# Kernel optimization log

Measured on AMD Instinct MI355X. Metric: run time of the kernel, lower is better.

## Reference

```python
import jax, jax.numpy as jnp
import numpy as np


def _rope(v, pos, head_dim):
    # v: [H, D]; rotate consecutive pairs by angle pos * theta_j
    theta = 1.0 / (10000.0 ** (jnp.arange(0, head_dim, 2, dtype=jnp.float32) / head_dim))
    ang = pos * theta                      # [D/2]
    cos, sin = jnp.cos(ang), jnp.sin(ang)
    vr = v.reshape(v.shape[0], -1, 2)      # [H, D/2, 2]
    re = vr[..., 0] * cos - vr[..., 1] * sin
    im = vr[..., 0] * sin + vr[..., 1] * cos
    return jnp.stack([re, im], axis=-1).reshape(v.shape)


def setup_inputs() -> dict:
    key = jax.random.key(0)
    ks = jax.random.split(key, 7)
    dim, H, D, S = 4096, 32, 128, 2048
    scale = 0.02
    return {
        "x": jax.random.normal(ks[0], (dim,), dtype=jnp.float32),
        "wq": jax.random.normal(ks[1], (dim, dim), dtype=jnp.float32) * scale,
        "wk": jax.random.normal(ks[2], (dim, dim), dtype=jnp.float32) * scale,
        "wv": jax.random.normal(ks[3], (dim, dim), dtype=jnp.float32) * scale,
        "wo": jax.random.normal(ks[4], (dim, dim), dtype=jnp.float32) * scale,
        "cache_k": jax.random.normal(ks[5], (S, H, D), dtype=jnp.float32),
        "cache_v": jax.random.normal(ks[6], (S, H, D), dtype=jnp.float32),
        "pos": 1536,
    }


def reference(x, wq, wk, wv, wo, cache_k, cache_v, pos):
    H, D = cache_k.shape[1], cache_k.shape[2]
    # nn.Linear without bias: y = W @ x
    xq = (wq @ x).reshape(H, D)
    xk = (wk @ x).reshape(H, D)
    xv = (wv @ x).reshape(H, D)
    xq = _rope(xq, pos, D)
    xk = _rope(xk, pos, D)
    # KV cache append (pos is a static Python int)
    cache_k = cache_k.at[pos].set(xk)
    cache_v = cache_v.at[pos].set(xv)
    keys = cache_k[: pos + 1]              # [P, H, D]
    values = cache_v[: pos + 1]            # [P, H, D]
    # single-query decode attention per head
    scores = jnp.einsum("hd,phd->hp", xq, keys) / jnp.sqrt(jnp.float32(D))
    scores = jax.nn.softmax(scores, axis=-1)
    out = jnp.einsum("hp,phd->hd", scores, values)   # [H, D]
    return wo @ out.reshape(-1)
```

## Files before the change

kernel.cpp:

```cpp
#include <hip/hip_runtime.h>
#include <math.h>

#define DIM 4096
#define H 32
#define D 128
#define SMAX 2048
#define CHUNK 32
#define NCHUNK (SMAX / CHUNK)
#define PART_STRIDE 130

typedef float v4f __attribute__((ext_vector_type(4)));
typedef unsigned int u32;

__device__ __forceinline__ float wave_sum(float v) {
#pragma unroll
    for (int o = 32; o; o >>= 1) v += __shfl_xor(v, o);
    return v;
}

__device__ __forceinline__ void gload_lds16(const float* g, float* l) {
    __builtin_amdgcn_global_load_lds(
        (const __attribute__((address_space(1))) u32*)g,
        (__attribute__((address_space(3))) u32*)l, 16, 0, 0);
}

__global__ void __launch_bounds__(256) qk_rope(
        const float* __restrict__ wq, const float* __restrict__ wk,
        const float* __restrict__ x, const int* __restrict__ pos_p,
        float* __restrict__ xq, float* __restrict__ xk) {
    __shared__ float buf[2 * DIM];
    __shared__ float red[2][4];
    int t = threadIdx.x, lane = t & 63, w = t >> 6;
    int bid = blockIdx.x;
    bool isq = bid < 2048;
    int pr = bid & 2047;
    const float* base = (isq ? wq : wk) + (size_t)pr * 2 * DIM;

    v4f xr[4];
#pragma unroll
    for (int i = 0; i < 4; ++i)
        xr[i] = *reinterpret_cast<const v4f*>(x + i * 1024 + t * 4);

#pragma unroll
    for (int i = 0; i < 8; ++i)
        gload_lds16(base + i * 1024 + t * 4, &buf[i * 1024 + t * 4]);

    __syncthreads();

    float a0 = 0.f, a1 = 0.f, a2 = 0.f, a3 = 0.f;
    float b0 = 0.f, b1 = 0.f, b2 = 0.f, b3 = 0.f;
#pragma unroll
    for (int i = 0; i < 4; ++i) {
        v4f ra = *reinterpret_cast<v4f*>(&buf[i * 1024 + t * 4]);
        v4f rb = *reinterpret_cast<v4f*>(&buf[DIM + i * 1024 + t * 4]);
        a0 = fmaf(ra.x, xr[i].x, a0);
        a1 = fmaf(ra.y, xr[i].y, a1);
        a2 = fmaf(ra.z, xr[i].z, a2);
        a3 = fmaf(ra.w, xr[i].w, a3);
        b0 = fmaf(rb.x, xr[i].x, b0);
        b1 = fmaf(rb.y, xr[i].y, b1);
        b2 = fmaf(rb.z, xr[i].z, b2);
        b3 = fmaf(rb.w, xr[i].w, b3);
    }
    float da = wave_sum((a0 + a1) + (a2 + a3));
    float db = wave_sum((b0 + b1) + (b2 + b3));
    if (lane == 0) { red[0][w] = da; red[1][w] = db; }
    __syncthreads();
    if (t == 0) {
        float d0 = red[0][0] + red[0][1] + red[0][2] + red[0][3];
        float d1 = red[1][0] + red[1][1] + red[1][2] + red[1][3];
        int pos = *pos_p;
        int j = pr & 63;
        float theta = powf(10000.0f, -(float)(2 * j) / (float)D);
        float ang = (float)pos * theta;
        float s, c;
        sincosf(ang, &s, &c);
        float* o = isq ? xq : xk;
        o[2 * pr]     = d0 * c - d1 * s;
        o[2 * pr + 1] = d0 * s + d1 * c;
    }
}

__global__ void __launch_bounds__(256) v_mat(
        const float* __restrict__ wv, const float* __restrict__ x,
        float* __restrict__ xv) {
    __shared__ float red[4];
    int row = blockIdx.x;
    const float* w = wv + (size_t)row * DIM;
    int t = threadIdx.x;
    float acc = 0.f;
#pragma unroll
    for (int i = 0; i < 4; ++i) {
        int idx = (i * 256 + t) * 4;
        const float4 a = *reinterpret_cast<const float4*>(w + idx);
        const float4 b = *reinterpret_cast<const float4*>(x + idx);
        acc = fmaf(a.x, b.x, acc);
        acc = fmaf(a.y, b.y, acc);
        acc = fmaf(a.z, b.z, acc);
        acc = fmaf(a.w, b.w, acc);
    }
#pragma unroll
    for (int off = 32; off; off >>= 1) acc += __shfl_xor(acc, off);
    if ((t & 63) == 0) red[t >> 6] = acc;
    __syncthreads();
    if (t == 0) xv[row] = red[0] + red[1] + red[2] + red[3];
}

__device__ __forceinline__ void load_half(v4f (&buf)[8], const float* __restrict__ wp, int off) {
#pragma unroll
    for (int i = 0; i < 8; ++i)
        buf[i] = *reinterpret_cast<const v4f*>(wp + i * 256 + off);
}

template <int XO>
__device__ __forceinline__ float dot_half(const v4f (&buf)[8], const v4f (&xr)[16]) {
    float s0 = 0.f, s1 = 0.f, s2 = 0.f, s3 = 0.f;
#pragma unroll
    for (int i = 0; i < 8; ++i) {
        s0 = fmaf(buf[i].x, xr[XO + i].x, s0);
        s1 = fmaf(buf[i].y, xr[XO + i].y, s1);
        s2 = fmaf(buf[i].z, xr[XO + i].z, s2);
        s3 = fmaf(buf[i].w, xr[XO + i].w, s3);
    }
    return (s0 + s1) + (s2 + s3);
}

#define SB() __builtin_amdgcn_sched_barrier(0)

__global__ void __launch_bounds__(256) matvec_o(
        const float* __restrict__ w_, const float* __restrict__ vin,
        float* __restrict__ y) {
    int t = threadIdx.x, lane = t & 63;
    int W = blockIdx.x * 4 + (t >> 6);
    int r0 = W * 2;
    int off = lane * 4;

    v4f xr[16];
#pragma unroll
    for (int i = 0; i < 16; ++i)
        xr[i] = *reinterpret_cast<const v4f*>(vin + i * 256 + off);

    const float* w0 = w_ + (size_t)r0 * DIM;
    v4f A[8], B[8];
    float d0, d1;
    load_half(A, w0, off);
    load_half(B, w0 + 2048, off);            SB();
    d0  = dot_half<0>(A, xr);
    load_half(A, w0 + DIM, off);             SB();
    d0 += dot_half<8>(B, xr);
    load_half(B, w0 + DIM + 2048, off);      SB();
    d1  = dot_half<0>(A, xr);
    d1 += dot_half<8>(B, xr);

    d0 = wave_sum(d0); d1 = wave_sum(d1);
    if (lane == 0) { y[r0] = d0; y[r0 + 1] = d1; }
}

__global__ void attn_partial(const float* __restrict__ cache_k, const float* __restrict__ cache_v,
                             const float* __restrict__ xq, const float* __restrict__ xk,
                             const float* __restrict__ xv, const int* __restrict__ pos_p,
                             float* __restrict__ partials) {
    __shared__ float lds_m[4], lds_l[4];
    __shared__ float lds_acc[4][128];
    int h = blockIdx.x;
    int c = blockIdx.y;
    int lane = threadIdx.x;
    int g  = lane >> 4;
    int gl = lane & 15;
    int pos = *pos_p;
    int base = c * CHUNK;
    int p1 = min(base + CHUNK, pos + 1);
    float* pp = partials + (size_t)(h * NCHUNK + c) * PART_STRIDE;

    if (base > pos) {
        if (lane == 0) { pp[0] = -INFINITY; pp[1] = 0.f; }
        reinterpret_cast<float2*>(pp + 2)[lane] = make_float2(0.f, 0.f);
        return;
    }

    const float4* qv = reinterpret_cast<const float4*>(xq + h * D + gl * 8);
    const float4 q0 = qv[0], q1 = qv[1];

    float m = -INFINITY, l = 0.f;
    float4 acc0 = make_float4(0.f, 0.f, 0.f, 0.f);
    float4 acc1 = make_float4(0.f, 0.f, 0.f, 0.f);

    for (int p = base + g; p < p1; p += 4) {
        const float* kp = (p == pos) ? (xk + h * D)
                                     : (cache_k + ((size_t)p * H + h) * D);
        const float4* kv4 = reinterpret_cast<const float4*>(kp + gl * 8);
        float4 k0 = kv4[0], k1 = kv4[1];
        float d = q0.x * k0.x + q0.y * k0.y + q0.z * k0.z + q0.w * k0.w
                + q1.x * k1.x + q1.y * k1.y + q1.z * k1.z + q1.w * k1.w;
        d += __shfl_xor(d, 1);
        d += __shfl_xor(d, 2);
        d += __shfl_xor(d, 4);
        d += __shfl_xor(d, 8);
        float s = d * 0.08838834764831845f;
        float mn = fmaxf(m, s);
        float corr = __expf(m - mn);
        float wgt  = __expf(s - mn);
        const float* vp = (p == pos) ? (xv + h * D)
                                     : (cache_v + ((size_t)p * H + h) * D);
        const float4* vv4 = reinterpret_cast<const float4*>(vp + gl * 8);
        float4 v0 = vv4[0], v1 = vv4[1];
        l = l * corr + wgt;
        acc0.x = fmaf(wgt, v0.x, acc0.x * corr);
        acc0.y = fmaf(wgt, v0.y, acc0.y * corr);
        acc0.z = fmaf(wgt, v0.z, acc0.z * corr);
        acc0.w = fmaf(wgt, v0.w, acc0.w * corr);
        acc1.x = fmaf(wgt, v1.x, acc1.x * corr);
        acc1.y = fmaf(wgt, v1.y, acc1.y * corr);
        acc1.z = fmaf(wgt, v1.z, acc1.z * corr);
        acc1.w = fmaf(wgt, v1.w, acc1.w * corr);
        m = mn;
    }

    if (gl == 0) { lds_m[g] = m; lds_l[g] = l; }
    *reinterpret_cast<float4*>(&lds_acc[g][gl * 8])     = acc0;
    *reinterpret_cast<float4*>(&lds_acc[g][gl * 8 + 4]) = acc1;
    __syncthreads();
    float M = fmaxf(fmaxf(lds_m[0], lds_m[1]), fmaxf(lds_m[2], lds_m[3]));
    float w0 = __expf(lds_m[0] - M);
    float w1 = __expf(lds_m[1] - M);
    float w2 = __expf(lds_m[2] - M);
    float w3 = __expf(lds_m[3] - M);
    float L  = w0 * lds_l[0] + w1 * lds_l[1] + w2 * lds_l[2] + w3 * lds_l[3];
    int d0 = 2 * lane;
    float s0 = w0 * lds_acc[0][d0]     + w1 * lds_acc[1][d0]
             + w2 * lds_acc[2][d0]     + w3 * lds_acc[3][d0];
    float s1 = w0 * lds_acc[0][d0 + 1] + w1 * lds_acc[1][d0 + 1]
             + w2 * lds_acc[2][d0 + 1] + w3 * lds_acc[3][d0 + 1];
    if (lane == 0) { pp[0] = M; pp[1] = L; }
    reinterpret_cast<float2*>(pp + 2)[lane] = make_float2(s0, s1);
}

__global__ void attn_combine(const float* __restrict__ partials, float* __restrict__ out_attn) {
    int h = blockIdx.x;
    int lane = threadIdx.x;
    float m = -INFINITY;
    for (int c = 0; c < NCHUNK; ++c)
        m = fmaxf(m, partials[(size_t)(h * NCHUNK + c) * PART_STRIDE]);
    float L = 0.f, a0 = 0.f, a1 = 0.f;
    for (int c = 0; c < NCHUNK; ++c) {
        const float* pp = partials + (size_t)(h * NCHUNK + c) * PART_STRIDE;
        float w = __expf(pp[0] - m);
        L += pp[1] * w;
        float2 a = reinterpret_cast<const float2*>(pp + 2)[lane];
        a0 += w * a.x;
        a1 += w * a.y;
    }
    float inv = 1.f / L;
    out_attn[h * D + 2 * lane]     = a0 * inv;
    out_attn[h * D + 2 * lane + 1] = a1 * inv;
}

extern "C" void kernel_launch(void* const* d_in, const int* in_sizes, int n_in,
                              void* d_out, int out_size, void* d_ws, size_t ws_size,
                              hipStream_t stream) {
    const float* x       = (const float*)d_in[0];
    const float* wq      = (const float*)d_in[1];
    const float* wk      = (const float*)d_in[2];
    const float* wv      = (const float*)d_in[3];
    const float* wo      = (const float*)d_in[4];
    const float* cache_k = (const float*)d_in[5];
    const float* cache_v = (const float*)d_in[6];
    const int*   pos     = (const int*)d_in[7];

    float* ws       = (float*)d_ws;
    float* xq       = ws;
    float* xk       = ws + DIM;
    float* xv       = ws + 2 * DIM;
    float* partials = ws + 3 * DIM;
    float* out_attn = partials + H * NCHUNK * PART_STRIDE;
    float* out      = (float*)d_out;

    qk_rope<<<4096, 256, 0, stream>>>(wq, wk, x, pos, xq, xk);
    v_mat<<<DIM, 256, 0, stream>>>(wv, x, xv);
    attn_partial<<<dim3(H, NCHUNK), 64, 0, stream>>>(cache_k, cache_v, xq, xk, xv, pos, partials);
    attn_combine<<<H, 64, 0, stream>>>(partials, out_attn);
    matvec_o<<<512, 256, 0, stream>>>(wo, out_attn, out);
}
```

Before: 78.56 us.

## Fuse decode pipeline into one cooperative persistent kernel with grid syncs

Replaces the five separate launches (QK-rope matvec, V matvec, attention partials, combine, output projection) with a single cooperative kernel of 1024 persistent blocks, with grid.sync between stages. The aim is to remove launch gaps and tail effects between stages. The partial layout is also moved so the accumulator sits at offset 0 and max/sum at 128/129. The change risks grid.sync overhead, lower occupancy under launch bounds, and a fallback to the old path if cooperative launch is unavailable.

Measured after the change: 78.79 us. No clear change (+0.3%).

```diff
diff --git a/kernel.cpp b/kernel.cpp
--- a/kernel.cpp
+++ b/kernel.cpp
@@ -1,5 +1,8 @@
 #include <hip/hip_runtime.h>
+#include <hip/hip_cooperative_groups.h>
 #include <math.h>
+
+namespace cg = cooperative_groups;
 
 #define DIM 4096
 #define H 32
@@ -7,7 +10,9 @@
 #define SMAX 2048
 #define CHUNK 32
 #define NCHUNK (SMAX / CHUNK)
-#define PART_STRIDE 130
+#define PART_STRIDE 132
+#define NBLK 1024
+#define NTHR 256
 
 typedef float v4f __attribute__((ext_vector_type(4)));
 typedef unsigned int u32;
@@ -16,6 +21,217 @@
 #pragma unroll
     for (int o = 32; o; o >>= 1) v += __shfl_xor(v, o);
     return v;
+}
+
+__device__ __forceinline__ void vsum1632(v4f& v) {
+#pragma unroll
+    for (int i = 0; i < 4; ++i) {
+        float f = v[i];
+        f += __shfl_xor(f, 16);
+        f += __shfl_xor(f, 32);
+        v[i] = f;
+    }
+}
+
+__global__ void __launch_bounds__(NTHR, 4) fused_decode(
+        const float* __restrict__ wq, const float* __restrict__ wk,
+        const float* __restrict__ wv, const float* __restrict__ wo,
+        const float* __restrict__ x,
+        const float* __restrict__ cache_k, const float* __restrict__ cache_v,
+        const int* __restrict__ pos_p,
+        float* __restrict__ xq, float* __restrict__ xk, float* __restrict__ xv,
+        float* __restrict__ partials, float* __restrict__ out_attn,
+        float* __restrict__ y) {
+    __shared__ float xs[DIM];
+    __shared__ float red[2][2][4];
+    cg::grid_group grid = cg::this_grid();
+
+    int t = threadIdx.x, lane = t & 63, w = t >> 6;
+    int bid = blockIdx.x;
+    int pos = *pos_p;
+
+#pragma unroll
+    for (int i = 0; i < 4; ++i)
+        *reinterpret_cast<v4f*>(&xs[(i * 256 + t) * 4]) =
+            *reinterpret_cast<const v4f*>(x + (i * 256 + t) * 4);
+    __syncthreads();
+
+    {
+        int par = 0;
+        for (int tp = bid; tp < 3 * 2048; tp += NBLK, par ^= 1) {
+            int mat = tp >> 11;
+            int pr  = tp & 2047;
+            const float* wm = (mat == 0) ? wq : ((mat == 1) ? wk : wv);
+            const float* base = wm + (size_t)pr * 2 * DIM;
+            v4f wa[4], wb[4];
+#pragma unroll
+            for (int i = 0; i < 4; ++i) {
+                wa[i] = *reinterpret_cast<const v4f*>(base + i * 1024 + t * 4);
+                wb[i] = *reinterpret_cast<const v4f*>(base + DIM + i * 1024 + t * 4);
+            }
+            float a0 = 0.f, a1 = 0.f, a2 = 0.f, a3 = 0.f;
+            float b0 = 0.f, b1 = 0.f, b2 = 0.f, b3 = 0.f;
+#pragma unroll
+            for (int i = 0; i < 4; ++i) {
+                v4f xr = *reinterpret_cast<const v4f*>(&xs[i * 1024 + t * 4]);
+                a0 = fmaf(wa[i].x, xr.x, a0);
+                a1 = fmaf(wa[i].y, xr.y, a1);
+                a2 = fmaf(wa[i].z, xr.z, a2);
+                a3 = fmaf(wa[i].w, xr.w, a3);
+                b0 = fmaf(wb[i].x, xr.x, b0);
+                b1 = fmaf(wb[i].y, xr.y, b1);
+                b2 = fmaf(wb[i].z, xr.z, b2);
+                b3 = fmaf(wb[i].w, xr.w, b3);
+            }
+            float da = wave_sum((a0 + a1) + (a2 + a3));
+            float db = wave_sum((b0 + b1) + (b2 + b3));
+            if (lane == 0) { red[par][0][w] = da; red[par][1][w] = db; }
+            __syncthreads();
+            if (t == 0) {
+                float d0 = red[par][0][0] + red[par][0][1] + red[par][0][2] + red[par][0][3];
+                float d1 = red[par][1][0] + red[par][1][1] + red[par][1][2] + red[par][1][3];
+                if (mat == 2) {
+                    xv[2 * pr] = d0; xv[2 * pr + 1] = d1;
+                } else {
+                    int j = pr & 63;
+                    float theta = powf(10000.0f, -(float)(2 * j) / (float)D);
+                    float ang = (float)pos * theta;
+                    float s, c;
+                    sincosf(ang, &s, &c);
+                    float* o = (mat == 0) ? xq : xk;
+                    o[2 * pr]     = d0 * c - d1 * s;
+                    o[2 * pr + 1] = d0 * s + d1 * c;
+                }
+            }
+        }
+    }
+    grid.sync();
+
+    {
+        int gid = bid * 4 + w;
+        int g = lane >> 4, gl = lane & 15;
+        for (int task = gid; task < H * NCHUNK; task += NBLK * 4) {
+            int h = task >> 6;
+            int c = task & 63;
+            int base_p = c * CHUNK;
+            float* pp = partials + (size_t)task * PART_STRIDE;
+
+            float m = -INFINITY, l = 0.f;
+            v4f acc0 = {0.f, 0.f, 0.f, 0.f}, acc1 = {0.f, 0.f, 0.f, 0.f};
+
+            if (base_p <= pos) {
+                v4f q0 = *reinterpret_cast<const v4f*>(xq + h * D + gl * 8);
+                v4f q1 = *reinterpret_cast<const v4f*>(xq + h * D + gl * 8 + 4);
+                int p1 = min(base_p + CHUNK, pos + 1);
+                for (int p = base_p + g; p < p1; p += 4) {
+                    const float* kp = (p == pos) ? (xk + h * D)
+                                                 : (cache_k + ((size_t)p * H + h) * D);
+                    v4f k0 = *reinterpret_cast<const v4f*>(kp + gl * 8);
+                    v4f k1 = *reinterpret_cast<const v4f*>(kp + gl * 8 + 4);
+                    float d = q0.x * k0.x + q0.y * k0.y + q0.z * k0.z + q0.w * k0.w
+                            + q1.x * k1.x + q1.y * k1.y + q1.z * k1.z + q1.w * k1.w;
+                    d += __shfl_xor(d, 1);
+                    d += __shfl_xor(d, 2);
+                    d += __shfl_xor(d, 4);
+                    d += __shfl_xor(d, 8);
+                    float s = d * 0.08838834764831845f;
+                    float mn = fmaxf(m, s);
+                    float corr = __expf(m - mn);
+                    float wgt  = __expf(s - mn);
+                    const float* vp = (p == pos) ? (xv + h * D)
+                                                 : (cache_v + ((size_t)p * H + h) * D);
+                    v4f v0 = *reinterpret_cast<const v4f*>(vp + gl * 8);
+                    v4f v1 = *reinterpret_cast<const v4f*>(vp + gl * 8 + 4);
+                    l = l * corr + wgt;
+                    acc0 = acc0 * corr + v0 * wgt;
+                    acc1 = acc1 * corr + v1 * wgt;
+                    m = mn;
+                }
+            }
+            float mm = fmaxf(m, __shfl_xor(m, 16));
+            float M  = fmaxf(mm, __shfl_xor(mm, 32));
+            float wg = (m == -INFINITY) ? 0.f : __expf(m - M);
+            float lw = l * wg;
+            lw += __shfl_xor(lw, 16);
+            lw += __shfl_xor(lw, 32);
+            acc0 = acc0 * wg;
+            acc1 = acc1 * wg;
+            vsum1632(acc0);
+            vsum1632(acc1);
+            if (lane == 0) { pp[128] = M; pp[129] = lw; }
+            if (lane < 16) {
+                *reinterpret_cast<v4f*>(pp + gl * 8)     = acc0;
+                *reinterpret_cast<v4f*>(pp + gl * 8 + 4) = acc1;
+            }
+        }
+    }
+    grid.sync();
+
+    {
+        int gid = bid * 4 + w;
+        if (gid < H) {
+            int h = gid;
+            float m = -INFINITY;
+            for (int c = 0; c < NCHUNK; ++c)
+                m = fmaxf(m, partials[(size_t)(h * NCHUNK + c) * PART_STRIDE + 128]);
+            float L = 0.f, a0 = 0.f, a1 = 0.f;
+            for (int c = 0; c < NCHUNK; ++c) {
+                const float* pp = partials + (size_t)(h * NCHUNK + c) * PART_STRIDE;
+                float mw = pp[128];
+                float wgt = (mw == -INFINITY) ? 0.f : __expf(mw - m);
+                L += pp[129] * wgt;
+                float2 a = *reinterpret_cast<const float2*>(pp + 2 * lane);
+                a0 += wgt * a.x;
+                a1 += wgt * a.y;
+            }
+            float inv = 1.f / L;
+            out_attn[h * D + 2 * lane]     = a0 * inv;
+            out_attn[h * D + 2 * lane + 1] = a1 * inv;
+        }
+    }
+    grid.sync();
+
+#pragma unroll
+    for (int i = 0; i < 4; ++i)
+        *reinterpret_cast<v4f*>(&xs[(i * 256 + t) * 4]) =
+            *reinterpret_cast<const v4f*>(out_attn + (i * 256 + t) * 4);
+    __syncthreads();
+    {
+        int par = 0;
+        for (int tp = bid; tp < 2048; tp += NBLK, par ^= 1) {
+            const float* base = wo + (size_t)tp * 2 * DIM;
+            v4f wa[4], wb[4];
+#pragma unroll
+            for (int i = 0; i < 4; ++i) {
+                wa[i] = *reinterpret_cast<const v4f*>(base + i * 1024 + t * 4);
+                wb[i] = *reinterpret_cast<const v4f*>(base + DIM + i * 1024 + t * 4);
+            }
+            float a0 = 0.f, a1 = 0.f, a2 = 0.f, a3 = 0.f;
+            float b0 = 0.f, b1 = 0.f, b2 = 0.f, b3 = 0.f;
+#pragma unroll
+            for (int i = 0; i < 4; ++i) {
+                v4f xr = *reinterpret_cast<const v4f*>(&xs[i * 1024 + t * 4]);
+                a0 = fmaf(wa[i].x, xr.x, a0);
+                a1 = fmaf(wa[i].y, xr.y, a1);
+                a2 = fmaf(wa[i].z, xr.z, a2);
+                a3 = fmaf(wa[i].w, xr.w, a3);
+                b0 = fmaf(wb[i].x, xr.x, b0);
+                b1 = fmaf(wb[i].y, xr.y, b1);
+                b2 = fmaf(wb[i].z, xr.z, b2);
+                b3 = fmaf(wb[i].w, xr.w, b3);
+            }
+            float da = wave_sum((a0 + a1) + (a2 + a3));
+            float db = wave_sum((b0 + b1) + (b2 + b3));
+            if (lane == 0) { red[par][0][w] = da; red[par][1][w] = db; }
+            __syncthreads();
+            if (t == 0) {
+                float d0 = red[par][0][0] + red[par][0][1] + red[par][0][2] + red[par][0][3];
+                float d1 = red[par][1][0] + red[par][1][1] + red[par][1][2] + red[par][1][3];
+                y[2 * tp]     = d0;
+                y[2 * tp + 1] = d1;
+            }
+        }
+    }
 }
 
 __device__ __forceinline__ void gload_lds16(const float* g, float* l) {
@@ -173,8 +389,8 @@
     float* pp = partials + (size_t)(h * NCHUNK + c) * PART_STRIDE;
 
     if (base > pos) {
-        if (lane == 0) { pp[0] = -INFINITY; pp[1] = 0.f; }
-        reinterpret_cast<float2*>(pp + 2)[lane] = make_float2(0.f, 0.f);
+        if (lane == 0) { pp[128] = -INFINITY; pp[129] = 0.f; }
+        reinterpret_cast<float2*>(pp)[lane] = make_float2(0.f, 0.f);
         return;
     }
 
@@ -231,8 +447,8 @@
              + w2 * lds_acc[2][d0]     + w3 * lds_acc[3][d0];
     float s1 = w0 * lds_acc[0][d0 + 1] + w1 * lds_acc[1][d0 + 1]
              + w2 * lds_acc[2][d0 + 1] + w3 * lds_acc[3][d0 + 1];
-    if (lane == 0) { pp[0] = M; pp[1] = L; }
-    reinterpret_cast<float2*>(pp + 2)[lane] = make_float2(s0, s1);
+    if (lane == 0) { pp[128] = M; pp[129] = L; }
+    reinterpret_cast<float2*>(pp)[lane] = make_float2(s0, s1);
 }
 
 __global__ void attn_combine(const float* __restrict__ partials, float* __restrict__ out_attn) {
@@ -240,13 +456,14 @@
     int lane = threadIdx.x;
     float m = -INFINITY;
     for (int c = 0; c < NCHUNK; ++c)
-        m = fmaxf(m, partials[(size_t)(h * NCHUNK + c) * PART_STRIDE]);
+        m = fmaxf(m, partials[(size_t)(h * NCHUNK + c) * PART_STRIDE + 128]);
     float L = 0.f, a0 = 0.f, a1 = 0.f;
     for (int c = 0; c < NCHUNK; ++c) {
         const float* pp = partials + (size_t)(h * NCHUNK + c) * PART_STRIDE;
-        float w = __expf(pp[0] - m);
-        L += pp[1] * w;
-        float2 a = reinterpret_cast<const float2*>(pp + 2)[lane];
+        float mw = pp[128];
+        float w = (mw == -INFINITY) ? 0.f : __expf(mw - m);
+        L += pp[129] * w;
+        float2 a = *reinterpret_cast<const float2*>(pp + 2 * lane);
         a0 += w * a.x;
         a1 += w * a.y;
     }
@@ -267,17 +484,36 @@
     const float* cache_v = (const float*)d_in[6];
     const int*   pos     = (const int*)d_in[7];
 
-    float* ws       = (float*)d_ws;
-    float* xq       = ws;
-    float* xk       = ws + DIM;
-    float* xv       = ws + 2 * DIM;
-    float* partials = ws + 3 * DIM;
+    float* wsf      = (float*)d_ws;
+    float* xq       = wsf;
+    float* xk       = wsf + DIM;
+    float* xv       = wsf + 2 * DIM;
+    float* partials = wsf + 3 * DIM;
     float* out_attn = partials + H * NCHUNK * PART_STRIDE;
-    float* out      = (float*)d_out;
+    float* y        = (float*)d_out;
+
+    int dev = 0;
+    hipGetDevice(&dev);
+    int coop_ok = 0, n_cu = 0, occ = 0;
+    hipDeviceGetAttribute(&coop_ok, hipDeviceAttributeCooperativeLaunch, dev);
+    hipDeviceGetAttribute(&n_cu, hipDeviceAttributeMultiprocessorCount, dev);
+    hipOccupancyMaxActiveBlocksPerMultiprocessor(&occ, fused_decode, NTHR, 0);
+
+    if (coop_ok && occ > 0 && (long)occ * n_cu >= NBLK) {
+        void* args[] = {
+            (void*)&wq, (void*)&wk, (void*)&wv, (void*)&wo, (void*)&x,
+            (void*)&cache_k, (void*)&cache_v, (void*)&pos,
+            (void*)&xq, (void*)&xk, (void*)&xv,
+            (void*)&partials, (void*)&out_attn, (void*)&y
+        };
+        hipError_t e = hipLaunchCooperativeKernel((const void*)fused_decode,
+                                                  dim3(NBLK), dim3(NTHR), args, 0, stream);
+        if (e == hipSuccess) return;
+    }
 
     qk_rope<<<4096, 256, 0, stream>>>(wq, wk, x, pos, xq, xk);
     v_mat<<<DIM, 256, 0, stream>>>(wv, x, xv);
     attn_partial<<<dim3(H, NCHUNK), 64, 0, stream>>>(cache_k, cache_v, xq, xk, xv, pos, partials);
     attn_combine<<<H, 64, 0, stream>>>(partials, out_attn);
-    matvec_o<<<512, 256, 0, stream>>>(wo, out_attn, out);
-}
+    matvec_o<<<512, 256, 0, stream>>>(wo, out_attn, y);
+}
```

## Fuse Q/K/V projections into one launch and realign attention partial layout

Applied to the files above, without the earlier changes.

Merges the V projection into the Q/K RoPE kernel, so one launch of 6144 blocks covers all three weight matrices, with two rows per block. Weights now go through direct global vector loads instead of the asynchronous global-to-LDS copy and shared buffer. The attention partial record is padded to 132 floats, with the accumulator first and max/sum stored after it, so the float2 accesses stay aligned. The combine step now skips chunks whose max is -inf. This removes a kernel launch and the LDS staging overhead, but loses the LDS prefetch path and any overlap it provided.

Measured after the change: 80.59 us. +2.6%, slower.

```diff
diff --git a/kernel.cpp b/kernel.cpp
--- a/kernel.cpp
+++ b/kernel.cpp
@@ -7,10 +7,9 @@
 #define SMAX 2048
 #define CHUNK 32
 #define NCHUNK (SMAX / CHUNK)
-#define PART_STRIDE 130
+#define PART_STRIDE 132
 
 typedef float v4f __attribute__((ext_vector_type(4)));
-typedef unsigned int u32;
 
 __device__ __forceinline__ float wave_sum(float v) {
 #pragma unroll
@@ -18,49 +17,35 @@
     return v;
 }
 
-__device__ __forceinline__ void gload_lds16(const float* g, float* l) {
-    __builtin_amdgcn_global_load_lds(
-        (const __attribute__((address_space(1))) u32*)g,
-        (__attribute__((address_space(3))) u32*)l, 16, 0, 0);
-}
-
-__global__ void __launch_bounds__(256) qk_rope(
+__global__ void __launch_bounds__(256) qkv_rope(
         const float* __restrict__ wq, const float* __restrict__ wk,
-        const float* __restrict__ x, const int* __restrict__ pos_p,
-        float* __restrict__ xq, float* __restrict__ xk) {
-    __shared__ float buf[2 * DIM];
+        const float* __restrict__ wv, const float* __restrict__ x,
+        const int* __restrict__ pos_p,
+        float* __restrict__ xq, float* __restrict__ xk, float* __restrict__ xv) {
     __shared__ float red[2][4];
     int t = threadIdx.x, lane = t & 63, w = t >> 6;
-    int bid = blockIdx.x;
-    bool isq = bid < 2048;
-    int pr = bid & 2047;
-    const float* base = (isq ? wq : wk) + (size_t)pr * 2 * DIM;
-
-    v4f xr[4];
-#pragma unroll
-    for (int i = 0; i < 4; ++i)
-        xr[i] = *reinterpret_cast<const v4f*>(x + i * 1024 + t * 4);
-
-#pragma unroll
-    for (int i = 0; i < 8; ++i)
-        gload_lds16(base + i * 1024 + t * 4, &buf[i * 1024 + t * 4]);
-
-    __syncthreads();
+    int b = blockIdx.x;
+    int mat = b >> 11;
+    int pr  = b & 2047;
+    const float* wm = (mat == 0) ? wq : ((mat == 1) ? wk : wv);
+    const float* base = wm + (size_t)pr * 2 * DIM;
 
     float a0 = 0.f, a1 = 0.f, a2 = 0.f, a3 = 0.f;
     float b0 = 0.f, b1 = 0.f, b2 = 0.f, b3 = 0.f;
 #pragma unroll
     for (int i = 0; i < 4; ++i) {
-        v4f ra = *reinterpret_cast<v4f*>(&buf[i * 1024 + t * 4]);
-        v4f rb = *reinterpret_cast<v4f*>(&buf[DIM + i * 1024 + t * 4]);
-        a0 = fmaf(ra.x, xr[i].x, a0);
-        a1 = fmaf(ra.y, xr[i].y, a1);
-        a2 = fmaf(ra.z, xr[i].z, a2);
-        a3 = fmaf(ra.w, xr[i].w, a3);
-        b0 = fmaf(rb.x, xr[i].x, b0);
-        b1 = fmaf(rb.y, xr[i].y, b1);
-        b2 = fmaf(rb.z, xr[i].z, b2);
-        b3 = fmaf(rb.w, xr[i].w, b3);
+        int idx = i * 1024 + t * 4;
+        v4f wa = *reinterpret_cast<const v4f*>(base + idx);
+        v4f wb = *reinterpret_cast<const v4f*>(base + DIM + idx);
+        v4f xr = *reinterpret_cast<const v4f*>(x + idx);
+        a0 = fmaf(wa.x, xr.x, a0);
+        a1 = fmaf(wa.y, xr.y, a1);
+        a2 = fmaf(wa.z, xr.z, a2);
+        a3 = fmaf(wa.w, xr.w, a3);
+        b0 = fmaf(wb.x, xr.x, b0);
+        b1 = fmaf(wb.y, xr.y, b1);
+        b2 = fmaf(wb.z, xr.z, b2);
+        b3 = fmaf(wb.w, xr.w, b3);
     }
     float da = wave_sum((a0 + a1) + (a2 + a3));
     float db = wave_sum((b0 + b1) + (b2 + b3));
@@ -69,91 +54,20 @@
     if (t == 0) {
         float d0 = red[0][0] + red[0][1] + red[0][2] + red[0][3];
         float d1 = red[1][0] + red[1][1] + red[1][2] + red[1][3];
-        int pos = *pos_p;
-        int j = pr & 63;
-        float theta = powf(10000.0f, -(float)(2 * j) / (float)D);
-        float ang = (float)pos * theta;
-        float s, c;
-        sincosf(ang, &s, &c);
-        float* o = isq ? xq : xk;
-        o[2 * pr]     = d0 * c - d1 * s;
-        o[2 * pr + 1] = d0 * s + d1 * c;
-    }
-}
-
-__global__ void __launch_bounds__(256) v_mat(
-        const float* __restrict__ wv, const float* __restrict__ x,
-        float* __restrict__ xv) {
-    __shared__ float red[4];
-    int row = blockIdx.x;
-    const float* w = wv + (size_t)row * DIM;
-    int t = threadIdx.x;
-    float acc = 0.f;
-#pragma unroll
-    for (int i = 0; i < 4; ++i) {
-        int idx = (i * 256 + t) * 4;
-        const float4 a = *reinterpret_cast<const float4*>(w + idx);
-        const float4 b = *reinterpret_cast<const float4*>(x + idx);
-        acc = fmaf(a.x, b.x, acc);
-        acc = fmaf(a.y, b.y, acc);
-        acc = fmaf(a.z, b.z, acc);
-        acc = fmaf(a.w, b.w, acc);
-    }
-#pragma unroll
-    for (int off = 32; off; off >>= 1) acc += __shfl_xor(acc, off);
-    if ((t & 63) == 0) red[t >> 6] = acc;
-    __syncthreads();
-    if (t == 0) xv[row] = red[0] + red[1] + red[2] + red[3];
-}
-
-__device__ __forceinline__ void load_half(v4f (&buf)[8], const float* __restrict__ wp, int off) {
-#pragma unroll
-    for (int i = 0; i < 8; ++i)
-        buf[i] = *reinterpret_cast<const v4f*>(wp + i * 256 + off);
-}
-
-template <int XO>
-__device__ __forceinline__ float dot_half(const v4f (&buf)[8], const v4f (&xr)[16]) {
-    float s0 = 0.f, s1 = 0.f, s2 = 0.f, s3 = 0.f;
-#pragma unroll
-    for (int i = 0; i < 8; ++i) {
-        s0 = fmaf(buf[i].x, xr[XO + i].x, s0);
-        s1 = fmaf(buf[i].y, xr[XO + i].y, s1);
-        s2 = fmaf(buf[i].z, xr[XO + i].z, s2);
-        s3 = fmaf(buf[i].w, xr[XO + i].w, s3);
-    }
-    return (s0 + s1) + (s2 + s3);
-}
-
-#define SB() __builtin_amdgcn_sched_barrier(0)
-
-__global__ void __launch_bounds__(256) matvec_o(
-        const float* __restrict__ w_, const float* __restrict__ vin,
-        float* __restrict__ y) {
-    int t = threadIdx.x, lane = t & 63;
-    int W = blockIdx.x * 4 + (t >> 6);
-    int r0 = W * 2;
-    int off = lane * 4;
-
-    v4f xr[16];
-#pragma unroll
-    for (int i = 0; i < 16; ++i)
-        xr[i] = *reinterpret_cast<const v4f*>(vin + i * 256 + off);
-
-    const float* w0 = w_ + (size_t)r0 * DIM;
-    v4f A[8], B[8];
-    float d0, d1;
-    load_half(A, w0, off);
-    load_half(B, w0 + 2048, off);            SB();
-    d0  = dot_half<0>(A, xr);
-    load_half(A, w0 + DIM, off);             SB();
-    d0 += dot_half<8>(B, xr);
-    load_half(B, w0 + DIM + 2048, off);      SB();
-    d1  = dot_half<0>(A, xr);
-    d1 += dot_half<8>(B, xr);
-
-    d0 = wave_sum(d0); d1 = wave_sum(d1);
-    if (lane == 0) { y[r0] = d0; y[r0 + 1] = d1; }
+        if (mat == 2) {
+            xv[2 * pr] = d0; xv[2 * pr + 1] = d1;
+        } else {
+            int pos = *pos_p;
+            int j = pr & 63;
+            float theta = powf(10000.0f, -(float)(2 * j) / (float)D);
+            float ang = (float)pos * theta;
+            float s, c;
+            sincosf(ang, &s, &c);
+            float* o = (mat == 0) ? xq : xk;
+            o[2 * pr]     = d0 * c - d1 * s;
+            o[2 * pr + 1] = d0 * s + d1 * c;
+        }
+    }
 }
 
 __global__ void attn_partial(const float* __restrict__ cache_k, const float* __restrict__ cache_v,
@@ -173,8 +87,8 @@
     float* pp = partials + (size_t)(h * NCHUNK + c) * PART_STRIDE;
 
     if (base > pos) {
-        if (lane == 0) { pp[0] = -INFINITY; pp[1] = 0.f; }
-        reinterpret_cast<float2*>(pp + 2)[lane] = make_float2(0.f, 0.f);
+        if (lane == 0) { pp[128] = -INFINITY; pp[129] = 0.f; }
+        reinterpret_cast<float2*>(pp)[lane] = make_float2(0.f, 0.f);
         return;
     }
 
@@ -231,8 +145,8 @@
              + w2 * lds_acc[2][d0]     + w3 * lds_acc[3][d0];
     float s1 = w0 * lds_acc[0][d0 + 1] + w1 * lds_acc[1][d0 + 1]
              + w2 * lds_acc[2][d0 + 1] + w3 * lds_acc[3][d0 + 1];
-    if (lane == 0) { pp[0] = M; pp[1] = L; }
-    reinterpret_cast<float2*>(pp + 2)[lane] = make_float2(s0, s1);
+    if (lane == 0) { pp[128] = M; pp[129] = L; }
+    reinterpret_cast<float2*>(pp)[lane] = make_float2(s0, s1);
 }
 
 __global__ void attn_combine(const float* __restrict__ partials, float* __restrict__ out_attn) {
@@ -240,19 +154,70 @@
     int lane = threadIdx.x;
     float m = -INFINITY;
     for (int c = 0; c < NCHUNK; ++c)
-        m = fmaxf(m, partials[(size_t)(h * NCHUNK + c) * PART_STRIDE]);
+        m = fmaxf(m, partials[(size_t)(h * NCHUNK + c) * PART_STRIDE + 128]);
     float L = 0.f, a0 = 0.f, a1 = 0.f;
     for (int c = 0; c < NCHUNK; ++c) {
         const float* pp = partials + (size_t)(h * NCHUNK + c) * PART_STRIDE;
-        float w = __expf(pp[0] - m);
-        L += pp[1] * w;
-        float2 a = reinterpret_cast<const float2*>(pp + 2)[lane];
+        float mw = pp[128];
+        float w = (mw == -INFINITY) ? 0.f : __expf(mw - m);
+        L += pp[129] * w;
+        float2 a = *reinterpret_cast<const float2*>(pp + 2 * lane);
         a0 += w * a.x;
         a1 += w * a.y;
     }
     float inv = 1.f / L;
     out_attn[h * D + 2 * lane]     = a0 * inv;
     out_attn[h * D + 2 * lane + 1] = a1 * inv;
+}
+
+__device__ __forceinline__ void load_half(v4f (&buf)[8], const float* __restrict__ wp, int off) {
+#pragma unroll
+    for (int i = 0; i < 8; ++i)
+        buf[i] = *reinterpret_cast<const v4f*>(wp + i * 256 + off);
+}
+
+template <int XO>
+__device__ __forceinline__ float dot_half(const v4f (&buf)[8], const v4f (&xr)[16]) {
+    float s0 = 0.f, s1 = 0.f, s2 = 0.f, s3 = 0.f;
+#pragma unroll
+    for (int i = 0; i < 8; ++i) {
+        s0 = fmaf(buf[i].x, xr[XO + i].x, s0);
+        s1 = fmaf(buf[i].y, xr[XO + i].y, s1);
+        s2 = fmaf(buf[i].z, xr[XO + i].z, s2);
+        s3 = fmaf(buf[i].w, xr[XO + i].w, s3);
+    }
+    return (s0 + s1) + (s2 + s3);
+}
+
+#define SB() __builtin_amdgcn_sched_barrier(0)
+
+__global__ void __launch_bounds__(256) matvec_o(
+        const float* __restrict__ w_, const float* __restrict__ vin,
+        float* __restrict__ y) {
+    int t = threadIdx.x, lane = t & 63;
+    int W = blockIdx.x * 4 + (t >> 6);
+    int r0 = W * 2;
+    int off = lane * 4;
+
+    v4f xr[16];
+#pragma unroll
+    for (int i = 0; i < 16; ++i)
+        xr[i] = *reinterpret_cast<const v4f*>(vin + i * 256 + off);
+
+    const float* w0 = w_ + (size_t)r0 * DIM;
+    v4f A[8], B[8];
+    float d0, d1;
+    load_half(A, w0, off);
+    load_half(B, w0 + 2048, off);            SB();
+    d0  = dot_half<0>(A, xr);
+    load_half(A, w0 + DIM, off);             SB();
+    d0 += dot_half<8>(B, xr);
+    load_half(B, w0 + DIM + 2048, off);      SB();
+    d1  = dot_half<0>(A, xr);
+    d1 += dot_half<8>(B, xr);
+
+    d0 = wave_sum(d0); d1 = wave_sum(d1);
+    if (lane == 0) { y[r0] = d0; y[r0 + 1] = d1; }
 }
 
 extern "C" void kernel_launch(void* const* d_in, const int* in_sizes, int n_in,
@@ -267,17 +232,16 @@
     const float* cache_v = (const float*)d_in[6];
     const int*   pos     = (const int*)d_in[7];
 
-    float* ws       = (float*)d_ws;
-    float* xq       = ws;
-    float* xk       = ws + DIM;
-    float* xv       = ws + 2 * DIM;
-    float* partials = ws + 3 * DIM;
+    float* wsf      = (float*)d_ws;
+    float* xq       = wsf;
+    float* xk       = wsf + DIM;
+    float* xv       = wsf + 2 * DIM;
+    float* partials = wsf + 3 * DIM;
     float* out_attn = partials + H * NCHUNK * PART_STRIDE;
-    float* out      = (float*)d_out;
-
-    qk_rope<<<4096, 256, 0, stream>>>(wq, wk, x, pos, xq, xk);
-    v_mat<<<DIM, 256, 0, stream>>>(wv, x, xv);
+    float* y        = (float*)d_out;
+
+    qkv_rope<<<3 * 2048, 256, 0, stream>>>(wq, wk, wv, x, pos, xq, xk, xv);
     attn_partial<<<dim3(H, NCHUNK), 64, 0, stream>>>(cache_k, cache_v, xq, xk, xv, pos, partials);
     attn_combine<<<H, 64, 0, stream>>>(partials, out_attn);
-    matvec_o<<<512, 256, 0, stream>>>(wo, out_attn, out);
-}
+    matvec_o<<<512, 256, 0, stream>>>(wo, out_attn, y);
+}
```
